# Kernel tuning notes

Hardware: AMD Instinct MI355X
Metric: run time of the kernel (lower is better)

## Reference

```python
import jax, jax.numpy as jnp
import numpy as np

EPS = 1e-5

def setup_inputs() -> dict:
    key = jax.random.key(0)
    k1, k2 = jax.random.split(key)
    N, D = 8192, 256
    q_features = jax.random.normal(k1, (N, D), dtype=jnp.float32)
    g_features = jax.random.normal(k2, (N, D), dtype=jnp.float32)
    return {"q_features": q_features, "g_features": g_features}

def reference(q_features, g_features):
    # logits[i, j] = q_i . g_j ; original computes row i as g_features @ q_i
    logits = jnp.einsum('id,jd->ij', q_features, g_features)  # [N, N]
    # exp(l_ii)/sum_j exp(l_ij) == softmax row diagonal (stable form, same math)
    probs_diag = jnp.diagonal(jax.nn.softmax(logits, axis=-1))  # [N]
    loss = jnp.mean(-jnp.log(probs_diag + EPS))
    return loss
```

## Files before the change

kernel.cpp:

```cpp
#include <hip/hip_runtime.h>
#include <stdint.h>


#define LOG2E 1.44269504f
#define KOFF  92.3324826f

typedef __attribute__((ext_vector_type(4))) float f32x4;
typedef __attribute__((ext_vector_type(4))) int   i32x4;
typedef __attribute__((ext_vector_type(8))) int   i32x8;

typedef __attribute__((address_space(1))) const uint32_t gu32;
typedef __attribute__((address_space(3))) uint32_t lu32;

static __device__ __forceinline__ i32x8 cat8(i32x4 lo, i32x4 hi) {
    i32x8 r;
    r[0] = lo[0]; r[1] = lo[1]; r[2] = lo[2]; r[3] = lo[3];
    r[4] = hi[0]; r[5] = hi[1]; r[6] = hi[2]; r[7] = hi[3];
    return r;
}

__global__ __launch_bounds__(256) void k_cvt(const float* __restrict__ q,
                                             const float* __restrict__ g,
                                             char* __restrict__ qb,
                                             char* __restrict__ gb,
                                             unsigned* __restrict__ counter) {
    if (blockIdx.x == 0 && threadIdx.x == 0) *counter = 0u;
    int o = blockIdx.x * 256 + threadIdx.x;
    const float* src = q;
    char* dst = qb;
    float sc = LOG2E;
    if (o >= 262144) { o -= 262144; src = g; dst = gb; sc = 1.0f; }
    int row = o >> 5, slot = o & 31;
    const float4* sp = (const float4*)(src + row * 256 + slot * 8);
    float4 a = sp[0], b = sp[1];
    uint32_t w0 = __builtin_amdgcn_cvt_pk_fp8_f32(a.x * sc, a.y * sc, 0, false);
    w0 = __builtin_amdgcn_cvt_pk_fp8_f32(a.z * sc, a.w * sc, w0, true);
    uint32_t w1 = __builtin_amdgcn_cvt_pk_fp8_f32(b.x * sc, b.y * sc, 0, false);
    w1 = __builtin_amdgcn_cvt_pk_fp8_f32(b.z * sc, b.w * sc, w1, true);
    int p = row >> 6, cf = (row >> 4) & 3, l15 = row & 15;
    int kb = slot >> 4;
    int gi = slot & 15;
    int quad = gi >> 2;
    int j = gi & 3;
    uint2 wv; wv.x = w0; wv.y = w1;
    *(uint2*)(dst + (size_t)p * 16384 + ((kb * 4 + cf) << 11)
              + ((j >> 1) << 10) + (quad * 16 + l15) * 16 + (j & 1) * 8) = wv;
}

__global__ __launch_bounds__(512, 2) void k_main(const char* __restrict__ qb,
                                                 const char* __restrict__ gb,
                                                 float* __restrict__ zpart,
                                                 float* __restrict__ diag) {
    __shared__ char lds[2][16384];
    const int tid  = threadIdx.x;
    const int wave = tid >> 6;
    const int lane = tid & 63;
    const int l15  = lane & 15;
    const int quad = lane >> 4;
    const int t    = blockIdx.x >> 5;
    const int cs   = blockIdx.x & 31;
    const int p64  = t * 8 + wave;
    const int rowbase = p64 * 64;

    i32x8 afrag[4][2];
    {
        const char* qp = qb + (size_t)p64 * 16384 + lane * 16;
#pragma unroll
        for (int rg = 0; rg < 4; ++rg)
#pragma unroll
            for (int kb = 0; kb < 2; ++kb) {
                const char* tp = qp + ((kb * 4 + rg) << 11);
                afrag[rg][kb] = cat8(*(const i32x4*)tp, *(const i32x4*)(tp + 1024));
            }
    }

    float zacc[4][4];
#pragma unroll
    for (int rg = 0; rg < 4; ++rg)
#pragma unroll
        for (int r = 0; r < 4; ++r) zacc[rg][r] = 0.f;

    const char* gbase = gb + (size_t)(cs * 4) * 16384;
#define STAGE(JT, BUF)                                                        \
    {                                                                         \
        const char* gp = gbase + (size_t)(JT) * 16384;                        \
        _Pragma("unroll")                                                     \
        for (int i = 0; i < 2; ++i) {                                         \
            int c = wave * 2 + i;                                             \
            __builtin_amdgcn_global_load_lds(                                 \
                (gu32*)(gp + (c << 10) + (lane << 4)),                        \
                (lu32*)(&lds[BUF][0] + (c << 10)), 16, 0, 0);                 \
        }                                                                     \
    }

    STAGE(0, 0);
    __syncthreads();
    int cur = 0;

    for (int jt = 0; jt < 4; ++jt) {
        if (jt < 3) STAGE(jt + 1, cur ^ 1);

        const bool dg = (cs * 4 + jt == p64);
        const char* lbase = &lds[cur][0] + lane * 16;
#pragma unroll 1
        for (int cf = 0; cf < 4; ++cf) {
            f32x4 acc[4];
#pragma unroll
            for (int rg = 0; rg < 4; ++rg)
                acc[rg] = (f32x4){-KOFF, -KOFF, -KOFF, -KOFF};
#pragma unroll
            for (int kb = 0; kb < 2; ++kb) {
                const char* bp = lbase + (cf << 11) + (kb << 13);
                i32x8 b = cat8(*(const i32x4*)bp, *(const i32x4*)(bp + 1024));
#pragma unroll
                for (int rg = 0; rg < 4; ++rg)
                    acc[rg] = __builtin_amdgcn_mfma_scale_f32_16x16x128_f8f6f4(
                        afrag[rg][kb], b, acc[rg],
                        0, 0,
                        0, 0x7f7f7f7f,
                        0, 0x7f7f7f7f);
            }
#pragma unroll
            for (int rg = 0; rg < 4; ++rg)
#pragma unroll
                for (int r = 0; r < 4; ++r)
                    zacc[rg][r] += __builtin_amdgcn_exp2f(acc[rg][r]);
            if (dg) {
#pragma unroll
                for (int rg = 0; rg < 4; ++rg)
                    if (rg == cf) {
#pragma unroll
                        for (int r = 0; r < 4; ++r)
                            if (quad * 4 + r == l15)
                                diag[rowbase + cf * 16 + l15] = acc[rg][r];
                    }
            }
        }
        if (jt < 3) {
            __syncthreads();
            cur ^= 1;
        }
    }
#undef STAGE

#pragma unroll
    for (int d = 1; d < 16; d <<= 1)
#pragma unroll
        for (int rg = 0; rg < 4; ++rg)
#pragma unroll
            for (int r = 0; r < 4; ++r)
                zacc[rg][r] += __shfl_xor(zacc[rg][r], d, 64);

    if (l15 == 0) {
#pragma unroll
        for (int rg = 0; rg < 4; ++rg)
#pragma unroll
            for (int r = 0; r < 4; ++r)
                zpart[(rowbase + rg * 16 + quad * 4 + r) * 32 + cs] = zacc[rg][r];
    }
}

__global__ __launch_bounds__(256) void k_fin(const float* __restrict__ zpart,
                                             const float* __restrict__ diag,
                                             float* __restrict__ partial,
                                             unsigned* __restrict__ counter,
                                             float* __restrict__ out) {
    __shared__ float red[4];
    __shared__ int lastflag;
    int r = blockIdx.x * 256 + threadIdx.x;
    const float4* z = (const float4*)(zpart + r * 32);
    float Z = 0.f;
#pragma unroll
    for (int i = 0; i < 8; ++i) {
        float4 a = z[i];
        Z += (a.x + a.y) + (a.z + a.w);
    }
    float p = __builtin_amdgcn_exp2f(diag[r]) / Z;
    float v = -logf(p + 1e-5f);
#pragma unroll
    for (int dd = 1; dd < 64; dd <<= 1) v += __shfl_xor(v, dd, 64);
    if ((threadIdx.x & 63) == 0) red[threadIdx.x >> 6] = v;
    __syncthreads();
    if (threadIdx.x == 0) {
        float bsum = (red[0] + red[1]) + (red[2] + red[3]);
        __hip_atomic_store(&partial[blockIdx.x], bsum,
                           __ATOMIC_RELAXED, __HIP_MEMORY_SCOPE_AGENT);
        __threadfence();
        lastflag = (atomicAdd(counter, 1u) == 31u);
    }
    __syncthreads();
    if (lastflag) {
        __threadfence();
        float v2 = 0.f;
        if (threadIdx.x < 32)
            v2 = __hip_atomic_load(&partial[threadIdx.x],
                                   __ATOMIC_RELAXED, __HIP_MEMORY_SCOPE_AGENT);
        if (threadIdx.x < 64) {
#pragma unroll
            for (int d = 1; d < 32; d <<= 1) v2 += __shfl_xor(v2, d, 64);
            if (threadIdx.x == 0) out[0] = v2 * (1.f / 8192.f);
        }
    }
}

extern "C" void kernel_launch(void* const* d_in, const int* in_sizes, int n_in,
                              void* d_out, int out_size, void* d_ws, size_t ws_size,
                              hipStream_t stream) {
    const float* q = (const float*)d_in[0];
    const float* g = (const float*)d_in[1];
    char* ws = (char*)d_ws;
    char*  qb     = ws;
    char*  gb     = ws + (2u << 20);
    float* diag   = (float*)(ws + (4u << 20));
    float* zpart  = (float*)(ws + (4u << 20) + (32u << 10));
    float* partial= (float*)(ws + (4u << 20) + (1056u << 10));
    unsigned* ctr = (unsigned*)(ws + (4u << 20) + (1056u << 10) + 128);
    k_cvt <<<2048, 256, 0, stream>>>(q, g, qb, gb, ctr);
    k_main<<<512,  512, 0, stream>>>(qb, gb, zpart, diag);
    k_fin <<<32,   256, 0, stream>>>(zpart, diag, partial, ctr, (float*)d_out);
    (void)in_sizes; (void)n_in; (void)out_size; (void)ws_size;
}
```

Baseline: 93.43 us.

## Fuse convert, GEMM-softmax and final reduction into one persistent kernel

Merges the three launches into a single kernel of 256 blocks that uses software grid barriers between the fp8 conversion phase, the MFMA logsumexp phase and the final reduction. Each block now covers two column slices (eight tiles) instead of one, halving the grid. The goal is to remove launch gaps and kernel boundaries. The barriers use monotonically increasing counters so they can be reused across calls, but they rely on all 256 blocks being co-resident and add spin-wait cost.

```diff
diff --git a/kernel.cpp b/kernel.cpp
--- a/kernel.cpp
+++ b/kernel.cpp
@@ -11,6 +11,8 @@
 
 typedef __attribute__((address_space(1))) const uint32_t gu32;
 typedef __attribute__((address_space(3))) uint32_t lu32;
+
+__device__ unsigned g_bar[4];
 
 static __device__ __forceinline__ i32x8 cat8(i32x4 lo, i32x4 hi) {
     i32x8 r;
@@ -19,46 +21,67 @@
     return r;
 }
 
-__global__ __launch_bounds__(256) void k_cvt(const float* __restrict__ q,
-                                             const float* __restrict__ g,
-                                             char* __restrict__ qb,
-                                             char* __restrict__ gb,
-                                             unsigned* __restrict__ counter) {
-    if (blockIdx.x == 0 && threadIdx.x == 0) *counter = 0u;
-    int o = blockIdx.x * 256 + threadIdx.x;
-    const float* src = q;
-    char* dst = qb;
-    float sc = LOG2E;
-    if (o >= 262144) { o -= 262144; src = g; dst = gb; sc = 1.0f; }
-    int row = o >> 5, slot = o & 31;
-    const float4* sp = (const float4*)(src + row * 256 + slot * 8);
-    float4 a = sp[0], b = sp[1];
-    uint32_t w0 = __builtin_amdgcn_cvt_pk_fp8_f32(a.x * sc, a.y * sc, 0, false);
-    w0 = __builtin_amdgcn_cvt_pk_fp8_f32(a.z * sc, a.w * sc, w0, true);
-    uint32_t w1 = __builtin_amdgcn_cvt_pk_fp8_f32(b.x * sc, b.y * sc, 0, false);
-    w1 = __builtin_amdgcn_cvt_pk_fp8_f32(b.z * sc, b.w * sc, w1, true);
-    int p = row >> 6, cf = (row >> 4) & 3, l15 = row & 15;
-    int kb = slot >> 4;
-    int gi = slot & 15;
-    int quad = gi >> 2;
-    int j = gi & 3;
-    uint2 wv; wv.x = w0; wv.y = w1;
-    *(uint2*)(dst + (size_t)p * 16384 + ((kb * 4 + cf) << 11)
-              + ((j >> 1) << 10) + (quad * 16 + l15) * 16 + (j & 1) * 8) = wv;
-}
-
-__global__ __launch_bounds__(512, 2) void k_main(const char* __restrict__ qb,
-                                                 const char* __restrict__ gb,
-                                                 float* __restrict__ zpart,
-                                                 float* __restrict__ diag) {
+static __device__ __forceinline__ void grid_barrier(unsigned* bar) {
+    __threadfence();
+    __syncthreads();
+    if (threadIdx.x == 0) {
+        unsigned my = __hip_atomic_fetch_add(bar, 1u, __ATOMIC_ACQ_REL,
+                                             __HIP_MEMORY_SCOPE_AGENT);
+        unsigned tgt = (my | 255u) + 1u;
+        while (__hip_atomic_load(bar, __ATOMIC_ACQUIRE,
+                                 __HIP_MEMORY_SCOPE_AGENT) < tgt)
+            __builtin_amdgcn_s_sleep(4);
+    }
+    __syncthreads();
+    __threadfence();
+}
+
+__global__ __launch_bounds__(512, 2) void k_all(const float* __restrict__ q,
+                                                const float* __restrict__ g,
+                                                char* __restrict__ qb,
+                                                char* __restrict__ gb,
+                                                float* __restrict__ zpart,
+                                                float* __restrict__ diag,
+                                                float* __restrict__ partial,
+                                                float* __restrict__ out) {
     __shared__ char lds[2][16384];
-    const int tid  = threadIdx.x;
+    __shared__ float red[8];
+    __shared__ int lastflag;
+    const int tid = threadIdx.x;
+
+    {
+        int gid = blockIdx.x * 512 + tid;
+#pragma unroll
+        for (int i = 0; i < 4; ++i) {
+            int o = i * 131072 + gid;
+            const float* src = q; char* dst = qb; float sc = LOG2E;
+            if (o >= 262144) { o -= 262144; src = g; dst = gb; sc = 1.0f; }
+            int row = o >> 5, slot = o & 31;
+            const float4* sp = (const float4*)(src + row * 256 + slot * 8);
+            float4 a = sp[0], b = sp[1];
+            uint32_t w0 = __builtin_amdgcn_cvt_pk_fp8_f32(a.x*sc, a.y*sc, 0, false);
+            w0 = __builtin_amdgcn_cvt_pk_fp8_f32(a.z*sc, a.w*sc, w0, true);
+            uint32_t w1 = __builtin_amdgcn_cvt_pk_fp8_f32(b.x*sc, b.y*sc, 0, false);
+            w1 = __builtin_amdgcn_cvt_pk_fp8_f32(b.z*sc, b.w*sc, w1, true);
+            int p = row >> 6, cfr = (row >> 4) & 3, l15r = row & 15;
+            int kb = slot >> 4;
+            int gi = slot & 15;
+            int qd = gi >> 2;
+            int j  = gi & 3;
+            uint2 wv; wv.x = w0; wv.y = w1;
+            *(uint2*)(dst + (size_t)p * 16384 + ((kb * 4 + cfr) << 11)
+                      + ((j >> 1) << 10) + (qd * 16 + l15r) * 16 + (j & 1) * 8) = wv;
+        }
+    }
+
+    grid_barrier(&g_bar[0]);
+
     const int wave = tid >> 6;
     const int lane = tid & 63;
     const int l15  = lane & 15;
     const int quad = lane >> 4;
-    const int t    = blockIdx.x >> 5;
-    const int cs   = blockIdx.x & 31;
+    const int t    = blockIdx.x >> 4;
+    const int cs0  = (blockIdx.x & 15) * 2;
     const int p64  = t * 8 + wave;
     const int rowbase = p64 * 64;
 
@@ -80,10 +103,10 @@
 #pragma unroll
         for (int r = 0; r < 4; ++r) zacc[rg][r] = 0.f;
 
-    const char* gbase = gb + (size_t)(cs * 4) * 16384;
-#define STAGE(JT, BUF)                                                        \
+    const char* gbase = gb + (size_t)(cs0 * 4) * 16384;
+#define STAGE(JJ, BUF)                                                        \
     {                                                                         \
-        const char* gp = gbase + (size_t)(JT) * 16384;                        \
+        const char* gp = gbase + (size_t)(JJ) * 16384;                        \
         _Pragma("unroll")                                                     \
         for (int i = 0; i < 2; ++i) {                                         \
             int c = wave * 2 + i;                                             \
@@ -97,10 +120,10 @@
     __syncthreads();
     int cur = 0;
 
-    for (int jt = 0; jt < 4; ++jt) {
-        if (jt < 3) STAGE(jt + 1, cur ^ 1);
-
-        const bool dg = (cs * 4 + jt == p64);
+    for (int jj = 0; jj < 8; ++jj) {
+        if (jj < 7) STAGE(jj + 1, cur ^ 1);
+
+        const bool dg = (cs0 * 4 + jj == p64);
         const char* lbase = &lds[cur][0] + lane * 16;
 #pragma unroll 1
         for (int cf = 0; cf < 4; ++cf) {
@@ -136,69 +159,78 @@
                     }
             }
         }
-        if (jt < 3) {
+
+        if (jj == 3 || jj == 7) {
+#pragma unroll
+            for (int d = 1; d < 16; d <<= 1)
+#pragma unroll
+                for (int rg = 0; rg < 4; ++rg)
+#pragma unroll
+                    for (int r = 0; r < 4; ++r)
+                        zacc[rg][r] += __shfl_xor(zacc[rg][r], d, 64);
+            if (l15 == 0) {
+                int cs = cs0 + (jj >> 2);
+#pragma unroll
+                for (int rg = 0; rg < 4; ++rg)
+#pragma unroll
+                    for (int r = 0; r < 4; ++r)
+                        zpart[(rowbase + rg * 16 + quad * 4 + r) * 32 + cs]
+                            = zacc[rg][r];
+            }
+#pragma unroll
+            for (int rg = 0; rg < 4; ++rg)
+#pragma unroll
+                for (int r = 0; r < 4; ++r) zacc[rg][r] = 0.f;
+        }
+
+        if (jj < 7) {
             __syncthreads();
             cur ^= 1;
         }
     }
 #undef STAGE
 
-#pragma unroll
-    for (int d = 1; d < 16; d <<= 1)
-#pragma unroll
-        for (int rg = 0; rg < 4; ++rg)
-#pragma unroll
-            for (int r = 0; r < 4; ++r)
-                zacc[rg][r] += __shfl_xor(zacc[rg][r], d, 64);
-
-    if (l15 == 0) {
-#pragma unroll
-        for (int rg = 0; rg < 4; ++rg)
-#pragma unroll
-            for (int r = 0; r < 4; ++r)
-                zpart[(rowbase + rg * 16 + quad * 4 + r) * 32 + cs] = zacc[rg][r];
-    }
-}
-
-__global__ __launch_bounds__(256) void k_fin(const float* __restrict__ zpart,
-                                             const float* __restrict__ diag,
-                                             float* __restrict__ partial,
-                                             unsigned* __restrict__ counter,
-                                             float* __restrict__ out) {
-    __shared__ float red[4];
-    __shared__ int lastflag;
-    int r = blockIdx.x * 256 + threadIdx.x;
-    const float4* z = (const float4*)(zpart + r * 32);
-    float Z = 0.f;
-#pragma unroll
-    for (int i = 0; i < 8; ++i) {
-        float4 a = z[i];
-        Z += (a.x + a.y) + (a.z + a.w);
-    }
-    float p = __builtin_amdgcn_exp2f(diag[r]) / Z;
-    float v = -logf(p + 1e-5f);
-#pragma unroll
-    for (int dd = 1; dd < 64; dd <<= 1) v += __shfl_xor(v, dd, 64);
-    if ((threadIdx.x & 63) == 0) red[threadIdx.x >> 6] = v;
-    __syncthreads();
-    if (threadIdx.x == 0) {
-        float bsum = (red[0] + red[1]) + (red[2] + red[3]);
-        __hip_atomic_store(&partial[blockIdx.x], bsum,
-                           __ATOMIC_RELAXED, __HIP_MEMORY_SCOPE_AGENT);
-        __threadfence();
-        lastflag = (atomicAdd(counter, 1u) == 31u);
-    }
-    __syncthreads();
-    if (lastflag) {
-        __threadfence();
-        float v2 = 0.f;
-        if (threadIdx.x < 32)
-            v2 = __hip_atomic_load(&partial[threadIdx.x],
-                                   __ATOMIC_RELAXED, __HIP_MEMORY_SCOPE_AGENT);
-        if (threadIdx.x < 64) {
-#pragma unroll
-            for (int d = 1; d < 32; d <<= 1) v2 += __shfl_xor(v2, d, 64);
-            if (threadIdx.x == 0) out[0] = v2 * (1.f / 8192.f);
+    grid_barrier(&g_bar[1]);
+
+    {
+        int row = blockIdx.x * 32 + (tid >> 4);
+        int cp  = tid & 15;
+        float2 zz = *(const float2*)(zpart + row * 32 + cp * 2);
+        float Zp = zz.x + zz.y;
+#pragma unroll
+        for (int d = 1; d < 16; d <<= 1) Zp += __shfl_xor(Zp, d, 64);
+        float v = 0.f;
+        if ((lane & 15) == 0) {
+            float p = __builtin_amdgcn_exp2f(diag[row]) / Zp;
+            v = -logf(p + 1e-5f);
+        }
+#pragma unroll
+        for (int d = 16; d < 64; d <<= 1) v += __shfl_xor(v, d, 64);
+        if (lane == 0) red[wave] = v;
+        __syncthreads();
+        if (tid == 0) {
+            float bsum = ((red[0] + red[1]) + (red[2] + red[3]))
+                       + ((red[4] + red[5]) + (red[6] + red[7]));
+            __hip_atomic_store(&partial[blockIdx.x], bsum,
+                               __ATOMIC_RELAXED, __HIP_MEMORY_SCOPE_AGENT);
+            __threadfence();
+            unsigned my = __hip_atomic_fetch_add(&g_bar[2], 1u, __ATOMIC_ACQ_REL,
+                                                 __HIP_MEMORY_SCOPE_AGENT);
+            lastflag = ((my & 255u) == 255u);
+        }
+        __syncthreads();
+        if (lastflag) {
+            __threadfence();
+            float v2 = 0.f;
+            if (tid < 256)
+                v2 = __hip_atomic_load(&partial[tid],
+                                       __ATOMIC_RELAXED, __HIP_MEMORY_SCOPE_AGENT);
+#pragma unroll
+            for (int d = 1; d < 64; d <<= 1) v2 += __shfl_xor(v2, d, 64);
+            if (tid < 256 && lane == 0) red[tid >> 6] = v2;
+            __syncthreads();
+            if (tid == 0)
+                out[0] = ((red[0] + red[1]) + (red[2] + red[3])) * (1.f / 8192.f);
         }
     }
 }
@@ -214,9 +246,7 @@
     float* diag   = (float*)(ws + (4u << 20));
     float* zpart  = (float*)(ws + (4u << 20) + (32u << 10));
     float* partial= (float*)(ws + (4u << 20) + (1056u << 10));
-    unsigned* ctr = (unsigned*)(ws + (4u << 20) + (1056u << 10) + 128);
-    k_cvt <<<2048, 256, 0, stream>>>(q, g, qb, gb, ctr);
-    k_main<<<512,  512, 0, stream>>>(qb, gb, zpart, diag);
-    k_fin <<<32,   256, 0, stream>>>(zpart, diag, partial, ctr, (float*)d_out);
+    k_all<<<256, 512, 0, stream>>>(q, g, qb, gb, zpart, diag, partial,
+                                   (float*)d_out);
     (void)in_sizes; (void)n_in; (void)out_size; (void)ws_size;
 }
```

New measurement: 299.8 us. 3.21x slower.

## Fuse final reduction into main kernel via atomic row sums and last-block finish

Applied to the files above, without the earlier changes.

Drops the separate finalize kernel. Each block now atomically adds its per-row partial sums into a global Zrow array, which the convert kernel zeroes. A global counter that is never reset (taken modulo 512) picks the last block, and that block computes the loss over all 8192 rows. This saves one kernel launch and the write and read of the partial-sum matrix. In exchange it adds float atomics, which make the result order-dependent, and leaves a serial tail where a single block does the whole final reduction.

```diff
diff --git a/kernel.cpp b/kernel.cpp
--- a/kernel.cpp
+++ b/kernel.cpp
@@ -11,6 +11,8 @@
 
 typedef __attribute__((address_space(1))) const uint32_t gu32;
 typedef __attribute__((address_space(3))) uint32_t lu32;
+
+__device__ unsigned g_ctr;
 
 static __device__ __forceinline__ i32x8 cat8(i32x4 lo, i32x4 hi) {
     i32x8 r;
@@ -23,8 +25,8 @@
                                              const float* __restrict__ g,
                                              char* __restrict__ qb,
                                              char* __restrict__ gb,
-                                             unsigned* __restrict__ counter) {
-    if (blockIdx.x == 0 && threadIdx.x == 0) *counter = 0u;
+                                             float* __restrict__ Zrow) {
+    if (blockIdx.x < 32) Zrow[blockIdx.x * 256 + threadIdx.x] = 0.f;
     int o = blockIdx.x * 256 + threadIdx.x;
     const float* src = q;
     char* dst = qb;
@@ -49,9 +51,12 @@
 
 __global__ __launch_bounds__(512, 2) void k_main(const char* __restrict__ qb,
                                                  const char* __restrict__ gb,
-                                                 float* __restrict__ zpart,
-                                                 float* __restrict__ diag) {
+                                                 float* __restrict__ Zrow,
+                                                 float* __restrict__ diag,
+                                                 float* __restrict__ out) {
     __shared__ char lds[2][16384];
+    __shared__ float red[8];
+    __shared__ int lastflag;
     const int tid  = threadIdx.x;
     const int wave = tid >> 6;
     const int lane = tid & 63;
@@ -156,50 +161,37 @@
         for (int rg = 0; rg < 4; ++rg)
 #pragma unroll
             for (int r = 0; r < 4; ++r)
-                zpart[(rowbase + rg * 16 + quad * 4 + r) * 32 + cs] = zacc[rg][r];
-    }
-}
-
-__global__ __launch_bounds__(256) void k_fin(const float* __restrict__ zpart,
-                                             const float* __restrict__ diag,
-                                             float* __restrict__ partial,
-                                             unsigned* __restrict__ counter,
-                                             float* __restrict__ out) {
-    __shared__ float red[4];
-    __shared__ int lastflag;
-    int r = blockIdx.x * 256 + threadIdx.x;
-    const float4* z = (const float4*)(zpart + r * 32);
-    float Z = 0.f;
-#pragma unroll
-    for (int i = 0; i < 8; ++i) {
-        float4 a = z[i];
-        Z += (a.x + a.y) + (a.z + a.w);
-    }
-    float p = __builtin_amdgcn_exp2f(diag[r]) / Z;
-    float v = -logf(p + 1e-5f);
-#pragma unroll
-    for (int dd = 1; dd < 64; dd <<= 1) v += __shfl_xor(v, dd, 64);
-    if ((threadIdx.x & 63) == 0) red[threadIdx.x >> 6] = v;
+                atomicAdd(&Zrow[rowbase + rg * 16 + quad * 4 + r], zacc[rg][r]);
+    }
+
+    __threadfence();
     __syncthreads();
-    if (threadIdx.x == 0) {
-        float bsum = (red[0] + red[1]) + (red[2] + red[3]);
-        __hip_atomic_store(&partial[blockIdx.x], bsum,
-                           __ATOMIC_RELAXED, __HIP_MEMORY_SCOPE_AGENT);
-        __threadfence();
-        lastflag = (atomicAdd(counter, 1u) == 31u);
+    if (tid == 0) {
+        unsigned my = __hip_atomic_fetch_add(&g_ctr, 1u, __ATOMIC_ACQ_REL,
+                                             __HIP_MEMORY_SCOPE_AGENT);
+        lastflag = ((my & 511u) == 511u);
     }
     __syncthreads();
     if (lastflag) {
         __threadfence();
-        float v2 = 0.f;
-        if (threadIdx.x < 32)
-            v2 = __hip_atomic_load(&partial[threadIdx.x],
-                                   __ATOMIC_RELAXED, __HIP_MEMORY_SCOPE_AGENT);
-        if (threadIdx.x < 64) {
-#pragma unroll
-            for (int d = 1; d < 32; d <<= 1) v2 += __shfl_xor(v2, d, 64);
-            if (threadIdx.x == 0) out[0] = v2 * (1.f / 8192.f);
+        float v = 0.f;
+#pragma unroll
+        for (int i = 0; i < 16; ++i) {
+            int row = i * 512 + tid;
+            float Z = __hip_atomic_load(&Zrow[row], __ATOMIC_RELAXED,
+                                        __HIP_MEMORY_SCOPE_AGENT);
+            float dv = __hip_atomic_load(&diag[row], __ATOMIC_RELAXED,
+                                         __HIP_MEMORY_SCOPE_AGENT);
+            float p = __builtin_amdgcn_exp2f(dv) / Z;
+            v += -logf(p + 1e-5f);
         }
+#pragma unroll
+        for (int d = 1; d < 64; d <<= 1) v += __shfl_xor(v, d, 64);
+        if (lane == 0) red[wave] = v;
+        __syncthreads();
+        if (tid == 0)
+            out[0] = (((red[0] + red[1]) + (red[2] + red[3]))
+                    + ((red[4] + red[5]) + (red[6] + red[7]))) * (1.f / 8192.f);
     }
 }
 
@@ -209,14 +201,11 @@
     const float* q = (const float*)d_in[0];
     const float* g = (const float*)d_in[1];
     char* ws = (char*)d_ws;
-    char*  qb     = ws;
-    char*  gb     = ws + (2u << 20);
-    float* diag   = (float*)(ws + (4u << 20));
-    float* zpart  = (float*)(ws + (4u << 20) + (32u << 10));
-    float* partial= (float*)(ws + (4u << 20) + (1056u << 10));
-    unsigned* ctr = (unsigned*)(ws + (4u << 20) + (1056u << 10) + 128);
-    k_cvt <<<2048, 256, 0, stream>>>(q, g, qb, gb, ctr);
-    k_main<<<512,  512, 0, stream>>>(qb, gb, zpart, diag);
-    k_fin <<<32,   256, 0, stream>>>(zpart, diag, partial, ctr, (float*)d_out);
+    char*  qb   = ws;
+    char*  gb   = ws + (2u << 20);
+    float* diag = (float*)(ws + (4u << 20));
+    float* Zrow = (float*)(ws + (4u << 20) + (32u << 10));
+    k_cvt <<<2048, 256, 0, stream>>>(q, g, qb, gb, Zrow);
+    k_main<<<512,  512, 0, stream>>>(qb, gb, Zrow, diag, (float*)d_out);
     (void)in_sizes; (void)n_in; (void)out_size; (void)ws_size;
 }
```

Measured after the change: 158.4 us. 69.6% more time.
